# Kernel tuning notes

Measured on AMD Instinct MI355X. Metric: run time of the kernel, lower is better.

## Reference

```python
import jax, jax.numpy as jnp
import numpy as np

HIDDEN = 1024
MOE_FF = 512
SHARED_FF = 2816
NUM_EXPERTS = 16
TOP_K = 2
NORM_TOPK = True


def setup_inputs() -> dict:
    key = jax.random.key(0)
    ks = jax.random.split(key, 8)
    s = 0.02
    return {
        "layer_input": jax.random.normal(ks[0], (1, 2048, HIDDEN), dtype=jnp.float32),
        "gate_w": jax.random.normal(ks[1], (NUM_EXPERTS, HIDDEN), dtype=jnp.float32) * s,
        # fused gate_up weight per expert, laid out for x @ W: [E, hidden, 2*moe_ff]
        "w_gate_up": jax.random.normal(ks[2], (NUM_EXPERTS, HIDDEN, 2 * MOE_FF), dtype=jnp.float32) * s,
        # down weight per expert, laid out for h @ W: [E, moe_ff, hidden]
        "w_down": jax.random.normal(ks[3], (NUM_EXPERTS, MOE_FF, HIDDEN), dtype=jnp.float32) * s,
        # shared expert (Qwen2MoeMLP): Linear weights stored torch-style [out, in]
        "shared_w_gate": jax.random.normal(ks[4], (SHARED_FF, HIDDEN), dtype=jnp.float32) * s,
        "shared_w_up": jax.random.normal(ks[5], (SHARED_FF, HIDDEN), dtype=jnp.float32) * s,
        "shared_w_down": jax.random.normal(ks[6], (HIDDEN, SHARED_FF), dtype=jnp.float32) * s,
        "shared_gate_w": jax.random.normal(ks[7], (1, HIDDEN), dtype=jnp.float32) * s,
    }


def reference(layer_input, gate_w, w_gate_up, w_down,
              shared_w_gate, shared_w_up, shared_w_down, shared_gate_w):
    B, S, D = layer_input.shape
    x = layer_input.reshape(-1, D)  # [N, D]
    N = x.shape[0]

    # shared expert: silu-gated MLP, scaled by per-token sigmoid gate
    shared = (jax.nn.silu(x @ shared_w_gate.T) * (x @ shared_w_up.T)) @ shared_w_down.T
    shared = shared * jax.nn.sigmoid(x @ shared_gate_w.T)  # [N, D]

    # router: softmax in float32, top-k, optional renorm
    logits = x @ gate_w.T  # [N, E]
    probs = jax.nn.softmax(logits.astype(jnp.float32), axis=-1)
    rw, sel = jax.lax.top_k(probs, TOP_K)  # [N, K]
    if NORM_TOPK:
        rw = rw / rw.sum(axis=-1, keepdims=True)
    rw = rw.astype(x.dtype)

    # dense combine weights: zero for unselected experts (equivalent to
    # the sort/dispatch + grouped-GEMM + weighted scatter-combine)
    combine = jnp.zeros((N, NUM_EXPERTS), x.dtype).at[jnp.arange(N)[:, None], sel].set(rw)

    # expert gate_up projection, SwiGLU, down projection, weighted combine
    gu = jnp.einsum('nd,edf->nef', x, w_gate_up)  # [N, E, 2*moe_ff]
    g, h = jnp.split(gu, 2, axis=-1)
    h = jax.nn.silu(g) * h  # [N, E, moe_ff]
    expert_out = jnp.einsum('nef,efd,ne->nd', h, w_down, combine)  # [N, D]

    out = expert_out + shared
    return out.reshape(B, S, D)
```

## Files before the change

kernel.cpp:

```cpp
#include <hip/hip_runtime.h>
#include <hip/hip_bf16.h>

typedef unsigned short ushort_t;
typedef __bf16 bf16x8 __attribute__((ext_vector_type(8)));
typedef float f32x4 __attribute__((ext_vector_type(4)));

#define N_TOK 2048
#define DH    1024
#define FF    512
#define SFF   2816
#define NE    16

#define BM 128
#define BN 64
#define BK 64
#define LDK 72

__device__ __forceinline__ ushort_t f2bf(float f) {
  unsigned int x = __float_as_uint(f);
  unsigned int lsb = (x >> 16) & 1u;
  x += 0x7fffu + lsb;
  return (ushort_t)(x >> 16);
}
__device__ __forceinline__ float bf2f(ushort_t u) {
  union { unsigned int i; float f; } v; v.i = ((unsigned int)u) << 16; return v.f;
}
__device__ __forceinline__ uint4 cvt8v(const float4 a, const float4 b) {
  union { ushort_t u[8]; uint4 v; } r;
  r.u[0] = f2bf(a.x); r.u[1] = f2bf(a.y); r.u[2] = f2bf(a.z); r.u[3] = f2bf(a.w);
  r.u[4] = f2bf(b.x); r.u[5] = f2bf(b.y); r.u[6] = f2bf(b.z); r.u[7] = f2bf(b.w);
  return r.v;
}
__device__ __forceinline__ uint4 ld_cvt8(const float* __restrict__ p) {
  float4 a = *(const float4*)p;
  float4 b = *(const float4*)(p + 4);
  return cvt8v(a, b);
}

__global__ void transpose_kernel(const float* __restrict__ WGU, const float* __restrict__ WDN,
                                 ushort_t* __restrict__ WGUB, ushort_t* __restrict__ WDNB) {
  __shared__ ushort_t tl[64][72];
  int bid = blockIdx.x;
  const float* src; ushort_t* dst; int K, N, kt, nt;
  if (bid < 4096) {
    int e = bid >> 8, rem = bid & 255; kt = rem >> 4; nt = rem & 15;
    src = WGU + (size_t)e * DH * (2 * FF); dst = WGUB + (size_t)e * (2 * FF) * DH;
    K = DH; N = 2 * FF;
  } else {
    int b2 = bid - 4096;
    int e = b2 >> 7, rem = b2 & 127; kt = rem >> 4; nt = rem & 15;
    src = WDN + (size_t)e * FF * DH; dst = WDNB + (size_t)e * DH * FF;
    K = FF; N = DH;
  }
  int t = threadIdx.x;
  int k0 = kt * 64, n0 = nt * 64;
  int r = t >> 2, c0 = (t & 3) * 16;
  const float* sp = src + (size_t)(k0 + r) * N + n0 + c0;
  #pragma unroll
  for (int q = 0; q < 4; ++q) {
    float4 v = *(const float4*)(sp + q * 4);
    tl[c0 + q * 4 + 0][r] = f2bf(v.x);
    tl[c0 + q * 4 + 1][r] = f2bf(v.y);
    tl[c0 + q * 4 + 2][r] = f2bf(v.z);
    tl[c0 + q * 4 + 3][r] = f2bf(v.w);
  }
  __syncthreads();
  ushort_t* dp = dst + (size_t)(n0 + r) * K + k0 + c0;
  *(uint4*)(dp)     = *(uint4*)&tl[r][c0];
  *(uint4*)(dp + 8) = *(uint4*)&tl[r][c0 + 8];
}

__global__ void router_kernel(const float* __restrict__ X, const float* __restrict__ GW,
                              const float* __restrict__ SGW,
                              int* __restrict__ sel, float* __restrict__ wtk,
                              float* __restrict__ sgate) {
  int wave = threadIdx.x >> 6, lane = threadIdx.x & 63;
  int n = blockIdx.x * 4 + wave;
  const float* x = X + (size_t)n * DH;
  int e = lane & 15, s = lane >> 4;
  const float* gw = GW + (size_t)e * DH;
  float lg = 0.f;
  for (int i = 0; i < 256; ++i) {
    int d = s * 256 + i;
    lg += x[d] * gw[d];
  }
  lg += __shfl_down(lg, 32);
  lg += __shfl_down(lg, 16);

  float gd = 0.f;
  #pragma unroll
  for (int i = 0; i < 16; ++i) {
    int d = lane * 16 + i;
    gd += x[d] * SGW[d];
  }
  #pragma unroll
  for (int off = 32; off >= 1; off >>= 1) gd += __shfl_down(gd, off);

  float l[16];
  #pragma unroll
  for (int i = 0; i < 16; ++i) l[i] = __shfl(lg, i);

  if (lane == 0) {
    int i1 = 0; float v1 = l[0];
    #pragma unroll
    for (int i = 1; i < 16; ++i) if (l[i] > v1) { v1 = l[i]; i1 = i; }
    int i2 = -1; float v2 = -1e30f;
    #pragma unroll
    for (int i = 0; i < 16; ++i) { if (i == i1) continue; if (l[i] > v2) { v2 = l[i]; i2 = i; } }
    float p2 = __expf(v2 - v1);
    float inv = 1.f / (1.f + p2);
    sel[n * 2 + 0] = i1; sel[n * 2 + 1] = i2;
    wtk[n * 2 + 0] = inv; wtk[n * 2 + 1] = p2 * inv;
    sgate[n] = 1.f / (1.f + __expf(-gd));
  }
}

__global__ void scatter_kernel(const int* __restrict__ sel,
                               int* __restrict__ toks, int* __restrict__ slot_of,
                               int* __restrict__ offs) {
  __shared__ int cnt[NE], bas[NE];
  int t = threadIdx.x;
  if (t < NE) cnt[t] = 0;
  __syncthreads();
  for (int i = t; i < N_TOK * 2; i += 256) atomicAdd(&cnt[sel[i]], 1);
  __syncthreads();
  if (t == 0) {
    int s = 0;
    for (int e = 0; e < NE; ++e) { bas[e] = s; offs[e] = s; s += cnt[e]; }
    offs[NE] = s;
  }
  __syncthreads();
  if (t < NE) cnt[t] = 0;
  __syncthreads();
  for (int i = t; i < N_TOK * 2; i += 256) {
    int e = sel[i];
    int p = atomicAdd(&cnt[e], 1);
    int slot = bas[e] + p;
    toks[slot] = i >> 1;
    slot_of[i] = slot;
  }
}

__global__ __launch_bounds__(256, 3) void gateup_kernel(
    const float* __restrict__ X, const ushort_t* __restrict__ WGUB,
    const float* __restrict__ SWG, const float* __restrict__ SWU,
    ushort_t* __restrict__ HX, ushort_t* __restrict__ HS,
    const int* __restrict__ toks, const int* __restrict__ offs) {
  __shared__ __align__(16) ushort_t As[BM][LDK];
  __shared__ __align__(16) ushort_t Bgs[BN][LDK];
  __shared__ __align__(16) ushort_t Bus[BN][LDK];
  const int K = DH, NT = K / BK;

  int bid = blockIdx.x;
  int t = threadIdx.x;
  int wave = t >> 6, lane = t & 63;
  int wm = wave & 1, wn = wave >> 1;
  int qd = lane >> 4, l16 = lane & 15;
  int sr = t >> 3, sc = (t & 7) * 8;

  f32x4 accg[4][2], accu[4][2];
  #pragma unroll
  for (int i = 0; i < 4; ++i)
    #pragma unroll
    for (int j = 0; j < 2; ++j) {
      accg[i][j] = (f32x4){0.f, 0.f, 0.f, 0.f};
      accu[i][j] = (f32x4){0.f, 0.f, 0.f, 0.f};
    }

  int m0, n0, M, base, is_exp;

  if (bid < 704) {
    is_exp = 0; base = 0; M = N_TOK;
    n0 = (bid % 44) * BN; m0 = (bid / 44) * BM;
    const float* arow[4];
    const float *bgrow[2], *burow[2];
    #pragma unroll
    for (int p = 0; p < 4; ++p)
      arow[p] = X + (size_t)(m0 + sr + 32 * p) * K + sc;
    #pragma unroll
    for (int p = 0; p < 2; ++p) {
      bgrow[p] = SWG + (size_t)(n0 + sr + 32 * p) * K + sc;
      burow[p] = SWU + (size_t)(n0 + sr + 32 * p) * K + sc;
    }
    uint4 ar[4], bgr[2], bur[2];
    #pragma unroll
    for (int p = 0; p < 4; ++p) ar[p] = ld_cvt8(arow[p]);
    #pragma unroll
    for (int p = 0; p < 2; ++p) { bgr[p] = ld_cvt8(bgrow[p]); bur[p] = ld_cvt8(burow[p]); }

    for (int kt = 0; kt < NT; ++kt) {
      #pragma unroll
      for (int p = 0; p < 4; ++p)
        *(uint4*)&As[sr + 32 * p][sc] = ar[p];
      #pragma unroll
      for (int p = 0; p < 2; ++p) {
        *(uint4*)&Bgs[sr + 32 * p][sc] = bgr[p];
        *(uint4*)&Bus[sr + 32 * p][sc] = bur[p];
      }
      __syncthreads();
      if (kt + 1 < NT) {
        int ko = (kt + 1) * BK;
        #pragma unroll
        for (int p = 0; p < 4; ++p) ar[p] = ld_cvt8(arow[p] + ko);
        #pragma unroll
        for (int p = 0; p < 2; ++p) { bgr[p] = ld_cvt8(bgrow[p] + ko); bur[p] = ld_cvt8(burow[p] + ko); }
      }
      #pragma unroll
      for (int ks = 0; ks < 2; ++ks) {
        int kk = ks * 32 + qd * 8;
        bf16x8 af[4], bgf[2], buf[2];
        #pragma unroll
        for (int i = 0; i < 4; ++i)
          af[i] = *(const bf16x8*)&As[wm * 64 + i * 16 + l16][kk];
        #pragma unroll
        for (int j = 0; j < 2; ++j) {
          bgf[j] = *(const bf16x8*)&Bgs[wn * 32 + j * 16 + l16][kk];
          buf[j] = *(const bf16x8*)&Bus[wn * 32 + j * 16 + l16][kk];
        }
        #pragma unroll
        for (int i = 0; i < 4; ++i)
          #pragma unroll
          for (int j = 0; j < 2; ++j) {
            accg[i][j] = __builtin_amdgcn_mfma_f32_16x16x32_bf16(af[i], bgf[j], accg[i][j], 0, 0, 0);
            accu[i][j] = __builtin_amdgcn_mfma_f32_16x16x32_bf16(af[i], buf[j], accu[i][j], 0, 0, 0);
          }
      }
      __syncthreads();
    }
  } else {
    is_exp = 1;
    int b2 = bid - 704;
    int e = b2 >> 7, rem = b2 & 127;
    n0 = (rem & 7) * BN; m0 = (rem >> 3) * BM;
    base = offs[e]; M = offs[e + 1] - base;
    if (m0 >= M) return;
    const ushort_t* Wt = WGUB + (size_t)e * (2 * FF) * DH;

    const float* arow[4];
    #pragma unroll
    for (int p = 0; p < 4; ++p) {
      int m = m0 + sr + 32 * p;
      int mm = m < M ? m : (M - 1);
      arow[p] = X + (size_t)toks[base + mm] * K + sc;
    }
    const ushort_t *bgrow[2], *burow[2];
    #pragma unroll
    for (int p = 0; p < 2; ++p) {
      bgrow[p] = Wt + (size_t)(n0 + sr + 32 * p) * DH + sc;
      burow[p] = Wt + (size_t)(FF + n0 + sr + 32 * p) * DH + sc;
    }

    uint4 ar[4], bgr[2], bur[2];
    #pragma unroll
    for (int p = 0; p < 4; ++p) ar[p] = ld_cvt8(arow[p]);
    #pragma unroll
    for (int p = 0; p < 2; ++p) { bgr[p] = *(const uint4*)bgrow[p]; bur[p] = *(const uint4*)burow[p]; }

    for (int kt = 0; kt < NT; ++kt) {
      #pragma unroll
      for (int p = 0; p < 4; ++p)
        *(uint4*)&As[sr + 32 * p][sc] = ar[p];
      #pragma unroll
      for (int p = 0; p < 2; ++p) {
        *(uint4*)&Bgs[sr + 32 * p][sc] = bgr[p];
        *(uint4*)&Bus[sr + 32 * p][sc] = bur[p];
      }
      __syncthreads();
      if (kt + 1 < NT) {
        int ko = (kt + 1) * BK;
        #pragma unroll
        for (int p = 0; p < 4; ++p) ar[p] = ld_cvt8(arow[p] + ko);
        #pragma unroll
        for (int p = 0; p < 2; ++p) { bgr[p] = *(const uint4*)(bgrow[p] + ko); bur[p] = *(const uint4*)(burow[p] + ko); }
      }
      #pragma unroll
      for (int ks = 0; ks < 2; ++ks) {
        int kk = ks * 32 + qd * 8;
        bf16x8 af[4], bgf[2], buf[2];
        #pragma unroll
        for (int i = 0; i < 4; ++i)
          af[i] = *(const bf16x8*)&As[wm * 64 + i * 16 + l16][kk];
        #pragma unroll
        for (int j = 0; j < 2; ++j) {
          bgf[j] = *(const bf16x8*)&Bgs[wn * 32 + j * 16 + l16][kk];
          buf[j] = *(const bf16x8*)&Bus[wn * 32 + j * 16 + l16][kk];
        }
        #pragma unroll
        for (int i = 0; i < 4; ++i)
          #pragma unroll
          for (int j = 0; j < 2; ++j) {
            accg[i][j] = __builtin_amdgcn_mfma_f32_16x16x32_bf16(af[i], bgf[j], accg[i][j], 0, 0, 0);
            accu[i][j] = __builtin_amdgcn_mfma_f32_16x16x32_bf16(af[i], buf[j], accu[i][j], 0, 0, 0);
          }
      }
      __syncthreads();
    }
  }

  #pragma unroll
  for (int i = 0; i < 4; ++i)
    #pragma unroll
    for (int r = 0; r < 4; ++r) {
      int row = wm * 64 + i * 16 + qd * 4 + r;
      #pragma unroll
      for (int j = 0; j < 2; ++j) {
        float g = accg[i][j][r], u = accu[i][j][r];
        float h = g / (1.f + __expf(-g)) * u;
        As[row][wn * 32 + j * 16 + l16] = f2bf(h);
      }
    }
  __syncthreads();
  if (is_exp) {
    #pragma unroll
    for (int p = 0; p < 4; ++p) {
      int m = m0 + sr + 32 * p;
      if (m < M)
        *(uint4*)(HX + (size_t)(base + m) * FF + n0 + sc) = *(uint4*)&As[sr + 32 * p][sc];
    }
  } else {
    #pragma unroll
    for (int p = 0; p < 4; ++p) {
      int m = m0 + sr + 32 * p;
      *(uint4*)(HS + (size_t)m * SFF + n0 + sc) = *(uint4*)&As[sr + 32 * p][sc];
    }
  }
}

__global__ __launch_bounds__(256, 4) void down_kernel(
    const ushort_t* __restrict__ HX, const ushort_t* __restrict__ HS,
    const ushort_t* __restrict__ WDNB, const float* __restrict__ SWD,
    ushort_t* __restrict__ SD0, ushort_t* __restrict__ SD1,
    ushort_t* __restrict__ EXPO, const int* __restrict__ offs) {
  __shared__ __align__(16) ushort_t As[BM][LDK];
  __shared__ __align__(16) ushort_t Bs[BN][LDK];

  int bid = blockIdx.x;
  int t = threadIdx.x;
  int wave = t >> 6, lane = t & 63;
  int wm = wave & 1, wn = wave >> 1;
  int qd = lane >> 4, l16 = lane & 15;
  int sr = t >> 3, sc = (t & 7) * 8;

  f32x4 c[4][2];
  #pragma unroll
  for (int i = 0; i < 4; ++i)
    #pragma unroll
    for (int j = 0; j < 2; ++j) c[i][j] = (f32x4){0.f, 0.f, 0.f, 0.f};

  int m0, n0, M, base_row;
  ushort_t* outp;

  if (bid < 512) {
    int kz = bid >> 8, rem = bid & 255;
    m0 = (rem >> 4) * BM; n0 = (rem & 15) * BN;
    M = N_TOK; base_row = 0;
    const int KC = SFF / 2, NT = KC / BK;
    int kb = kz * KC;
    outp = kz ? SD1 : SD0;

    const ushort_t* arow[4];
    const float* brow[2];
    #pragma unroll
    for (int p = 0; p < 4; ++p)
      arow[p] = HS + (size_t)(m0 + sr + 32 * p) * SFF + kb + sc;
    #pragma unroll
    for (int p = 0; p < 2; ++p)
      brow[p] = SWD + (size_t)(n0 + sr + 32 * p) * SFF + kb + sc;

    uint4 ar[4], br[2];
    #pragma unroll
    for (int p = 0; p < 4; ++p) ar[p] = *(const uint4*)(arow[p]);
    #pragma unroll
    for (int p = 0; p < 2; ++p) br[p] = ld_cvt8(brow[p]);

    for (int kt = 0; kt < NT; ++kt) {
      #pragma unroll
      for (int p = 0; p < 4; ++p)
        *(uint4*)&As[sr + 32 * p][sc] = ar[p];
      #pragma unroll
      for (int p = 0; p < 2; ++p)
        *(uint4*)&Bs[sr + 32 * p][sc] = br[p];
      __syncthreads();
      if (kt + 1 < NT) {
        int ko = (kt + 1) * BK;
        #pragma unroll
        for (int p = 0; p < 4; ++p) ar[p] = *(const uint4*)(arow[p] + ko);
        #pragma unroll
        for (int p = 0; p < 2; ++p) br[p] = ld_cvt8(brow[p] + ko);
      }
      #pragma unroll
      for (int ks = 0; ks < 2; ++ks) {
        int kk = ks * 32 + qd * 8;
        bf16x8 af[4], bf[2];
        #pragma unroll
        for (int i = 0; i < 4; ++i)
          af[i] = *(const bf16x8*)&As[wm * 64 + i * 16 + l16][kk];
        #pragma unroll
        for (int j = 0; j < 2; ++j)
          bf[j] = *(const bf16x8*)&Bs[wn * 32 + j * 16 + l16][kk];
        #pragma unroll
        for (int i = 0; i < 4; ++i)
          #pragma unroll
          for (int j = 0; j < 2; ++j)
            c[i][j] = __builtin_amdgcn_mfma_f32_16x16x32_bf16(af[i], bf[j], c[i][j], 0, 0, 0);
      }
      __syncthreads();
    }
  } else {
    int b2 = bid - 512;
    int e = b2 >> 8, rem = b2 & 255;
    n0 = (rem & 15) * BN; m0 = (rem >> 4) * BM;
    int base = offs[e];
    M = offs[e + 1] - base;
    if (m0 >= M) return;
    base_row = base;
    const int NT = FF / BK;
    const ushort_t* Wd = WDNB + (size_t)e * DH * FF;
    const ushort_t* A = HX + (size_t)base * FF;
    outp = EXPO;

    const ushort_t* arow[4];
    #pragma unroll
    for (int p = 0; p < 4; ++p) {
      int m = m0 + sr + 32 * p;
      int mm = m < M ? m : (M - 1);
      arow[p] = A + (size_t)mm * FF + sc;
    }
    const ushort_t* brow[2];
    #pragma unroll
    for (int p = 0; p < 2; ++p)
      brow[p] = Wd + (size_t)(n0 + sr + 32 * p) * FF + sc;

    uint4 ar[4], br[2];
    #pragma unroll
    for (int p = 0; p < 4; ++p) ar[p] = *(const uint4*)(arow[p]);
    #pragma unroll
    for (int p = 0; p < 2; ++p) br[p] = *(const uint4*)(brow[p]);

    for (int kt = 0; kt < NT; ++kt) {
      #pragma unroll
      for (int p = 0; p < 4; ++p)
        *(uint4*)&As[sr + 32 * p][sc] = ar[p];
      #pragma unroll
      for (int p = 0; p < 2; ++p)
        *(uint4*)&Bs[sr + 32 * p][sc] = br[p];
      __syncthreads();
      if (kt + 1 < NT) {
        int ko = (kt + 1) * BK;
        #pragma unroll
        for (int p = 0; p < 4; ++p) ar[p] = *(const uint4*)(arow[p] + ko);
        #pragma unroll
        for (int p = 0; p < 2; ++p) br[p] = *(const uint4*)(brow[p] + ko);
      }
      #pragma unroll
      for (int ks = 0; ks < 2; ++ks) {
        int kk = ks * 32 + qd * 8;
        bf16x8 af[4], bf[2];
        #pragma unroll
        for (int i = 0; i < 4; ++i)
          af[i] = *(const bf16x8*)&As[wm * 64 + i * 16 + l16][kk];
        #pragma unroll
        for (int j = 0; j < 2; ++j)
          bf[j] = *(const bf16x8*)&Bs[wn * 32 + j * 16 + l16][kk];
        #pragma unroll
        for (int i = 0; i < 4; ++i)
          #pragma unroll
          for (int j = 0; j < 2; ++j)
            c[i][j] = __builtin_amdgcn_mfma_f32_16x16x32_bf16(af[i], bf[j], c[i][j], 0, 0, 0);
      }
      __syncthreads();
    }
  }

  #pragma unroll
  for (int i = 0; i < 4; ++i)
    #pragma unroll
    for (int r = 0; r < 4; ++r) {
      int row = wm * 64 + i * 16 + qd * 4 + r;
      #pragma unroll
      for (int j = 0; j < 2; ++j)
        As[row][wn * 32 + j * 16 + l16] = f2bf(c[i][j][r]);
    }
  __syncthreads();
  #pragma unroll
  for (int p = 0; p < 4; ++p) {
    int m = m0 + sr + 32 * p;
    if (m < M)
      *(uint4*)(outp + (size_t)(base_row + m) * DH + n0 + sc) = *(uint4*)&As[sr + 32 * p][sc];
  }
}

__global__ void combine_kernel(const ushort_t* __restrict__ SD0, const ushort_t* __restrict__ SD1,
                               const ushort_t* __restrict__ EXPO,
                               const float* __restrict__ sgate, const float* __restrict__ wtk,
                               const int* __restrict__ slot_of, float* __restrict__ out) {
  int n = blockIdx.x, t = threadIdx.x;
  float sg = sgate[n];
  float w0 = wtk[n * 2 + 0], w1 = wtk[n * 2 + 1];
  int s0 = slot_of[n * 2 + 0], s1 = slot_of[n * 2 + 1];
  int col = t * 4;
  ushort4 d0 = *(const ushort4*)(SD0 + (size_t)n * DH + col);
  ushort4 d1 = *(const ushort4*)(SD1 + (size_t)n * DH + col);
  ushort4 a  = *(const ushort4*)(EXPO + (size_t)s0 * DH + col);
  ushort4 b  = *(const ushort4*)(EXPO + (size_t)s1 * DH + col);
  float4 o;
  o.x = sg * (bf2f(d0.x) + bf2f(d1.x)) + w0 * bf2f(a.x) + w1 * bf2f(b.x);
  o.y = sg * (bf2f(d0.y) + bf2f(d1.y)) + w0 * bf2f(a.y) + w1 * bf2f(b.y);
  o.z = sg * (bf2f(d0.z) + bf2f(d1.z)) + w0 * bf2f(a.z) + w1 * bf2f(b.z);
  o.w = sg * (bf2f(d0.w) + bf2f(d1.w)) + w0 * bf2f(a.w) + w1 * bf2f(b.w);
  *(float4*)(out + (size_t)n * DH + col) = o;
}

extern "C" void kernel_launch(void* const* d_in, const int* in_sizes, int n_in,
                              void* d_out, int out_size, void* d_ws, size_t ws_size,
                              hipStream_t stream) {
  const float* x    = (const float*)d_in[0];
  const float* gw   = (const float*)d_in[1];
  const float* wgu  = (const float*)d_in[2];
  const float* wdn  = (const float*)d_in[3];
  const float* swg  = (const float*)d_in[4];
  const float* swu  = (const float*)d_in[5];
  const float* swd  = (const float*)d_in[6];
  const float* sgw  = (const float*)d_in[7];
  float* out = (float*)d_out;

  char* ws = (char*)d_ws;
  constexpr size_t OFF_HS   = 0;
  constexpr size_t OFF_HX   = OFF_HS   + (size_t)N_TOK * SFF * 2;
  constexpr size_t OFF_SD0  = OFF_HX   + (size_t)4096 * FF * 2;
  constexpr size_t OFF_SD1  = OFF_SD0  + (size_t)N_TOK * DH * 2;
  constexpr size_t OFF_EXPO = OFF_SD1  + (size_t)N_TOK * DH * 2;
  constexpr size_t OFF_WGUB = OFF_EXPO + (size_t)4096 * DH * 2;
  constexpr size_t OFF_WDNB = OFF_WGUB + (size_t)NE * (2 * FF) * DH * 2;
  constexpr size_t OFF_TOK  = OFF_WDNB + (size_t)NE * DH * FF * 2;
  constexpr size_t OFF_OFFS = OFF_TOK  + 4096 * 4;
  constexpr size_t OFF_SEL  = OFF_OFFS + 32 * 4;
  constexpr size_t OFF_WTK  = OFF_SEL  + 4096 * 4;
  constexpr size_t OFF_SG   = OFF_WTK  + 4096 * 4;
  constexpr size_t OFF_SLOT = OFF_SG   + 2048 * 4;

  ushort_t* hs    = (ushort_t*)(ws + OFF_HS);
  ushort_t* hx    = (ushort_t*)(ws + OFF_HX);
  ushort_t* sd0   = (ushort_t*)(ws + OFF_SD0);
  ushort_t* sd1   = (ushort_t*)(ws + OFF_SD1);
  ushort_t* expo  = (ushort_t*)(ws + OFF_EXPO);
  ushort_t* wgub  = (ushort_t*)(ws + OFF_WGUB);
  ushort_t* wdnb  = (ushort_t*)(ws + OFF_WDNB);
  int*      toks  = (int*)(ws + OFF_TOK);
  int*      offs  = (int*)(ws + OFF_OFFS);
  int*      sel   = (int*)(ws + OFF_SEL);
  float*    wtk   = (float*)(ws + OFF_WTK);
  float*    sgate = (float*)(ws + OFF_SG);
  int*      slot_of = (int*)(ws + OFF_SLOT);

  transpose_kernel<<<4096 + 2048, 256, 0, stream>>>(wgu, wdn, wgub, wdnb);
  router_kernel<<<N_TOK / 4, 256, 0, stream>>>(x, gw, sgw, sel, wtk, sgate);
  scatter_kernel<<<1, 256, 0, stream>>>(sel, toks, slot_of, offs);
  gateup_kernel<<<704 + 2048, 256, 0, stream>>>(x, wgub, swg, swu, hx, hs, toks, offs);
  down_kernel<<<512 + 4096, 256, 0, stream>>>(hx, hs, wdnb, swd, sd0, sd1, expo, offs);
  combine_kernel<<<N_TOK, 256, 0, stream>>>(sd0, sd1, expo, sgate, wtk, slot_of, out);
}
```

Baseline: 460.1 us.

## Pre-convert activations and shared weights to bf16; use nontemporal stores

Adds a convert kernel that casts X and the three shared-expert weight matrices to bf16 once, so the GEMM kernels load bf16 directly instead of reading fp32 and converting in every tile. The old code re-read fp32 X and the shared weights many times across tiles. The gateup kernel's two paths are merged into one main loop. Intermediate and output stores become nontemporal. In exchange it adds an extra kernel launch, a full fp32 read plus bf16 write pass, and more workspace.

```diff
diff --git a/kernel.cpp b/kernel.cpp
--- a/kernel.cpp
+++ b/kernel.cpp
@@ -4,6 +4,7 @@
 typedef unsigned short ushort_t;
 typedef __bf16 bf16x8 __attribute__((ext_vector_type(8)));
 typedef float f32x4 __attribute__((ext_vector_type(4)));
+typedef unsigned int u32x4 __attribute__((ext_vector_type(4)));
 
 #define N_TOK 2048
 #define DH    1024
@@ -35,6 +36,25 @@
   float4 a = *(const float4*)p;
   float4 b = *(const float4*)(p + 4);
   return cvt8v(a, b);
+}
+__device__ __forceinline__ void nt_store(ushort_t* p, uint4 v) {
+  union { uint4 h; u32x4 n; } u; u.h = v;
+  __builtin_nontemporal_store(u.n, (u32x4*)p);
+}
+
+__global__ void convert_kernel(const float* __restrict__ X, const float* __restrict__ SWG,
+                               const float* __restrict__ SWU, const float* __restrict__ SWD,
+                               ushort_t* __restrict__ XB, ushort_t* __restrict__ SWGB,
+                               ushort_t* __restrict__ SWUB, ushort_t* __restrict__ SWDB) {
+  const int NX = N_TOK * DH / 8;
+  const int NS = SFF * DH / 8;
+  int i = blockIdx.x * 256 + threadIdx.x;
+  const float* s; ushort_t* d; int off;
+  if (i < NX)               { s = X;   d = XB;   off = i; }
+  else if (i < NX + NS)     { s = SWG; d = SWGB; off = i - NX; }
+  else if (i < NX + 2 * NS) { s = SWU; d = SWUB; off = i - NX - NS; }
+  else                      { s = SWD; d = SWDB; off = i - NX - 2 * NS; }
+  nt_store(d + (size_t)off * 8, ld_cvt8(s + (size_t)off * 8));
 }
 
 __global__ void transpose_kernel(const float* __restrict__ WGU, const float* __restrict__ WDN,
@@ -66,8 +86,8 @@
   }
   __syncthreads();
   ushort_t* dp = dst + (size_t)(n0 + r) * K + k0 + c0;
-  *(uint4*)(dp)     = *(uint4*)&tl[r][c0];
-  *(uint4*)(dp + 8) = *(uint4*)&tl[r][c0 + 8];
+  nt_store(dp,     *(uint4*)&tl[r][c0]);
+  nt_store(dp + 8, *(uint4*)&tl[r][c0 + 8]);
 }
 
 __global__ void router_kernel(const float* __restrict__ X, const float* __restrict__ GW,
@@ -142,8 +162,8 @@
 }
 
 __global__ __launch_bounds__(256, 3) void gateup_kernel(
-    const float* __restrict__ X, const ushort_t* __restrict__ WGUB,
-    const float* __restrict__ SWG, const float* __restrict__ SWU,
+    const ushort_t* __restrict__ XB, const ushort_t* __restrict__ WGUB,
+    const ushort_t* __restrict__ SWGB, const ushort_t* __restrict__ SWUB,
     ushort_t* __restrict__ HX, ushort_t* __restrict__ HS,
     const int* __restrict__ toks, const int* __restrict__ offs) {
   __shared__ __align__(16) ushort_t As[BM][LDK];
@@ -168,64 +188,19 @@
     }
 
   int m0, n0, M, base, is_exp;
+  const ushort_t* arow[4];
+  const ushort_t *bgrow[2], *burow[2];
 
   if (bid < 704) {
     is_exp = 0; base = 0; M = N_TOK;
     n0 = (bid % 44) * BN; m0 = (bid / 44) * BM;
-    const float* arow[4];
-    const float *bgrow[2], *burow[2];
     #pragma unroll
     for (int p = 0; p < 4; ++p)
-      arow[p] = X + (size_t)(m0 + sr + 32 * p) * K + sc;
+      arow[p] = XB + (size_t)(m0 + sr + 32 * p) * K + sc;
     #pragma unroll
     for (int p = 0; p < 2; ++p) {
-      bgrow[p] = SWG + (size_t)(n0 + sr + 32 * p) * K + sc;
-      burow[p] = SWU + (size_t)(n0 + sr + 32 * p) * K + sc;
-    }
-    uint4 ar[4], bgr[2], bur[2];
-    #pragma unroll
-    for (int p = 0; p < 4; ++p) ar[p] = ld_cvt8(arow[p]);
-    #pragma unroll
-    for (int p = 0; p < 2; ++p) { bgr[p] = ld_cvt8(bgrow[p]); bur[p] = ld_cvt8(burow[p]); }
-
-    for (int kt = 0; kt < NT; ++kt) {
-      #pragma unroll
-      for (int p = 0; p < 4; ++p)
-        *(uint4*)&As[sr + 32 * p][sc] = ar[p];
-      #pragma unroll
-      for (int p = 0; p < 2; ++p) {
-        *(uint4*)&Bgs[sr + 32 * p][sc] = bgr[p];
-        *(uint4*)&Bus[sr + 32 * p][sc] = bur[p];
-      }
-      __syncthreads();
-      if (kt + 1 < NT) {
-        int ko = (kt + 1) * BK;
-        #pragma unroll
-        for (int p = 0; p < 4; ++p) ar[p] = ld_cvt8(arow[p] + ko);
-        #pragma unroll
-        for (int p = 0; p < 2; ++p) { bgr[p] = ld_cvt8(bgrow[p] + ko); bur[p] = ld_cvt8(burow[p] + ko); }
-      }
-      #pragma unroll
-      for (int ks = 0; ks < 2; ++ks) {
-        int kk = ks * 32 + qd * 8;
-        bf16x8 af[4], bgf[2], buf[2];
-        #pragma unroll
-        for (int i = 0; i < 4; ++i)
-          af[i] = *(const bf16x8*)&As[wm * 64 + i * 16 + l16][kk];
-        #pragma unroll
-        for (int j = 0; j < 2; ++j) {
-          bgf[j] = *(const bf16x8*)&Bgs[wn * 32 + j * 16 + l16][kk];
-          buf[j] = *(const bf16x8*)&Bus[wn * 32 + j * 16 + l16][kk];
-        }
-        #pragma unroll
-        for (int i = 0; i < 4; ++i)
-          #pragma unroll
-          for (int j = 0; j < 2; ++j) {
-            accg[i][j] = __builtin_amdgcn_mfma_f32_16x16x32_bf16(af[i], bgf[j], accg[i][j], 0, 0, 0);
-            accu[i][j] = __builtin_amdgcn_mfma_f32_16x16x32_bf16(af[i], buf[j], accu[i][j], 0, 0, 0);
-          }
-      }
-      __syncthreads();
+      bgrow[p] = SWGB + (size_t)(n0 + sr + 32 * p) * K + sc;
+      burow[p] = SWUB + (size_t)(n0 + sr + 32 * p) * K + sc;
     }
   } else {
     is_exp = 1;
@@ -235,66 +210,63 @@
     base = offs[e]; M = offs[e + 1] - base;
     if (m0 >= M) return;
     const ushort_t* Wt = WGUB + (size_t)e * (2 * FF) * DH;
-
-    const float* arow[4];
     #pragma unroll
     for (int p = 0; p < 4; ++p) {
       int m = m0 + sr + 32 * p;
       int mm = m < M ? m : (M - 1);
-      arow[p] = X + (size_t)toks[base + mm] * K + sc;
-    }
-    const ushort_t *bgrow[2], *burow[2];
+      arow[p] = XB + (size_t)toks[base + mm] * K + sc;
+    }
     #pragma unroll
     for (int p = 0; p < 2; ++p) {
       bgrow[p] = Wt + (size_t)(n0 + sr + 32 * p) * DH + sc;
       burow[p] = Wt + (size_t)(FF + n0 + sr + 32 * p) * DH + sc;
     }
-
-    uint4 ar[4], bgr[2], bur[2];
-    #pragma unroll
-    for (int p = 0; p < 4; ++p) ar[p] = ld_cvt8(arow[p]);
-    #pragma unroll
-    for (int p = 0; p < 2; ++p) { bgr[p] = *(const uint4*)bgrow[p]; bur[p] = *(const uint4*)burow[p]; }
-
-    for (int kt = 0; kt < NT; ++kt) {
-      #pragma unroll
-      for (int p = 0; p < 4; ++p)
-        *(uint4*)&As[sr + 32 * p][sc] = ar[p];
-      #pragma unroll
-      for (int p = 0; p < 2; ++p) {
-        *(uint4*)&Bgs[sr + 32 * p][sc] = bgr[p];
-        *(uint4*)&Bus[sr + 32 * p][sc] = bur[p];
+  }
+
+  uint4 ar[4], bgr[2], bur[2];
+  #pragma unroll
+  for (int p = 0; p < 4; ++p) ar[p] = *(const uint4*)arow[p];
+  #pragma unroll
+  for (int p = 0; p < 2; ++p) { bgr[p] = *(const uint4*)bgrow[p]; bur[p] = *(const uint4*)burow[p]; }
+
+  for (int kt = 0; kt < NT; ++kt) {
+    #pragma unroll
+    for (int p = 0; p < 4; ++p)
+      *(uint4*)&As[sr + 32 * p][sc] = ar[p];
+    #pragma unroll
+    for (int p = 0; p < 2; ++p) {
+      *(uint4*)&Bgs[sr + 32 * p][sc] = bgr[p];
+      *(uint4*)&Bus[sr + 32 * p][sc] = bur[p];
+    }
+    __syncthreads();
+    if (kt + 1 < NT) {
+      int ko = (kt + 1) * BK;
+      #pragma unroll
+      for (int p = 0; p < 4; ++p) ar[p] = *(const uint4*)(arow[p] + ko);
+      #pragma unroll
+      for (int p = 0; p < 2; ++p) { bgr[p] = *(const uint4*)(bgrow[p] + ko); bur[p] = *(const uint4*)(burow[p] + ko); }
+    }
+    #pragma unroll
+    for (int ks = 0; ks < 2; ++ks) {
+      int kk = ks * 32 + qd * 8;
+      bf16x8 af[4], bgf[2], buf[2];
+      #pragma unroll
+      for (int i = 0; i < 4; ++i)
+        af[i] = *(const bf16x8*)&As[wm * 64 + i * 16 + l16][kk];
+      #pragma unroll
+      for (int j = 0; j < 2; ++j) {
+        bgf[j] = *(const bf16x8*)&Bgs[wn * 32 + j * 16 + l16][kk];
+        buf[j] = *(const bf16x8*)&Bus[wn * 32 + j * 16 + l16][kk];
       }
-      __syncthreads();
-      if (kt + 1 < NT) {
-        int ko = (kt + 1) * BK;
-        #pragma unroll
-        for (int p = 0; p < 4; ++p) ar[p] = ld_cvt8(arow[p] + ko);
-        #pragma unroll
-        for (int p = 0; p < 2; ++p) { bgr[p] = *(const uint4*)(bgrow[p] + ko); bur[p] = *(const uint4*)(burow[p] + ko); }
-      }
-      #pragma unroll
-      for (int ks = 0; ks < 2; ++ks) {
-        int kk = ks * 32 + qd * 8;
-        bf16x8 af[4], bgf[2], buf[2];
-        #pragma unroll
-        for (int i = 0; i < 4; ++i)
-          af[i] = *(const bf16x8*)&As[wm * 64 + i * 16 + l16][kk];
+      #pragma unroll
+      for (int i = 0; i < 4; ++i)
         #pragma unroll
         for (int j = 0; j < 2; ++j) {
-          bgf[j] = *(const bf16x8*)&Bgs[wn * 32 + j * 16 + l16][kk];
-          buf[j] = *(const bf16x8*)&Bus[wn * 32 + j * 16 + l16][kk];
+          accg[i][j] = __builtin_amdgcn_mfma_f32_16x16x32_bf16(af[i], bgf[j], accg[i][j], 0, 0, 0);
+          accu[i][j] = __builtin_amdgcn_mfma_f32_16x16x32_bf16(af[i], buf[j], accu[i][j], 0, 0, 0);
         }
-        #pragma unroll
-        for (int i = 0; i < 4; ++i)
-          #pragma unroll
-          for (int j = 0; j < 2; ++j) {
-            accg[i][j] = __builtin_amdgcn_mfma_f32_16x16x32_bf16(af[i], bgf[j], accg[i][j], 0, 0, 0);
-            accu[i][j] = __builtin_amdgcn_mfma_f32_16x16x32_bf16(af[i], buf[j], accu[i][j], 0, 0, 0);
-          }
-      }
-      __syncthreads();
-    }
+    }
+    __syncthreads();
   }
 
   #pragma unroll
@@ -315,20 +287,20 @@
     for (int p = 0; p < 4; ++p) {
       int m = m0 + sr + 32 * p;
       if (m < M)
-        *(uint4*)(HX + (size_t)(base + m) * FF + n0 + sc) = *(uint4*)&As[sr + 32 * p][sc];
+        nt_store(HX + (size_t)(base + m) * FF + n0 + sc, *(uint4*)&As[sr + 32 * p][sc]);
     }
   } else {
     #pragma unroll
     for (int p = 0; p < 4; ++p) {
       int m = m0 + sr + 32 * p;
-      *(uint4*)(HS + (size_t)m * SFF + n0 + sc) = *(uint4*)&As[sr + 32 * p][sc];
+      nt_store(HS + (size_t)m * SFF + n0 + sc, *(uint4*)&As[sr + 32 * p][sc]);
     }
   }
 }
 
 __global__ __launch_bounds__(256, 4) void down_kernel(
     const ushort_t* __restrict__ HX, const ushort_t* __restrict__ HS,
-    const ushort_t* __restrict__ WDNB, const float* __restrict__ SWD,
+    const ushort_t* __restrict__ WDNB, const ushort_t* __restrict__ SWDB,
     ushort_t* __restrict__ SD0, ushort_t* __restrict__ SD1,
     ushort_t* __restrict__ EXPO, const int* __restrict__ offs) {
   __shared__ __align__(16) ushort_t As[BM][LDK];
@@ -359,19 +331,19 @@
     outp = kz ? SD1 : SD0;
 
     const ushort_t* arow[4];
-    const float* brow[2];
+    const ushort_t* brow[2];
     #pragma unroll
     for (int p = 0; p < 4; ++p)
       arow[p] = HS + (size_t)(m0 + sr + 32 * p) * SFF + kb + sc;
     #pragma unroll
     for (int p = 0; p < 2; ++p)
-      brow[p] = SWD + (size_t)(n0 + sr + 32 * p) * SFF + kb + sc;
+      brow[p] = SWDB + (size_t)(n0 + sr + 32 * p) * SFF + kb + sc;
 
     uint4 ar[4], br[2];
     #pragma unroll
     for (int p = 0; p < 4; ++p) ar[p] = *(const uint4*)(arow[p]);
     #pragma unroll
-    for (int p = 0; p < 2; ++p) br[p] = ld_cvt8(brow[p]);
+    for (int p = 0; p < 2; ++p) br[p] = *(const uint4*)(brow[p]);
 
     for (int kt = 0; kt < NT; ++kt) {
       #pragma unroll
@@ -386,7 +358,7 @@
         #pragma unroll
         for (int p = 0; p < 4; ++p) ar[p] = *(const uint4*)(arow[p] + ko);
         #pragma unroll
-        for (int p = 0; p < 2; ++p) br[p] = ld_cvt8(brow[p] + ko);
+        for (int p = 0; p < 2; ++p) br[p] = *(const uint4*)(brow[p] + ko);
       }
       #pragma unroll
       for (int ks = 0; ks < 2; ++ks) {
@@ -486,7 +458,7 @@
   for (int p = 0; p < 4; ++p) {
     int m = m0 + sr + 32 * p;
     if (m < M)
-      *(uint4*)(outp + (size_t)(base_row + m) * DH + n0 + sc) = *(uint4*)&As[sr + 32 * p][sc];
+      nt_store(outp + (size_t)(base_row + m) * DH + n0 + sc, *(uint4*)&As[sr + 32 * p][sc]);
   }
 }
 
@@ -532,7 +504,11 @@
   constexpr size_t OFF_EXPO = OFF_SD1  + (size_t)N_TOK * DH * 2;
   constexpr size_t OFF_WGUB = OFF_EXPO + (size_t)4096 * DH * 2;
   constexpr size_t OFF_WDNB = OFF_WGUB + (size_t)NE * (2 * FF) * DH * 2;
-  constexpr size_t OFF_TOK  = OFF_WDNB + (size_t)NE * DH * FF * 2;
+  constexpr size_t OFF_XB   = OFF_WDNB + (size_t)NE * DH * FF * 2;
+  constexpr size_t OFF_SWGB = OFF_XB   + (size_t)N_TOK * DH * 2;
+  constexpr size_t OFF_SWUB = OFF_SWGB + (size_t)SFF * DH * 2;
+  constexpr size_t OFF_SWDB = OFF_SWUB + (size_t)SFF * DH * 2;
+  constexpr size_t OFF_TOK  = OFF_SWDB + (size_t)SFF * DH * 2;
   constexpr size_t OFF_OFFS = OFF_TOK  + 4096 * 4;
   constexpr size_t OFF_SEL  = OFF_OFFS + 32 * 4;
   constexpr size_t OFF_WTK  = OFF_SEL  + 4096 * 4;
@@ -546,6 +522,10 @@
   ushort_t* expo  = (ushort_t*)(ws + OFF_EXPO);
   ushort_t* wgub  = (ushort_t*)(ws + OFF_WGUB);
   ushort_t* wdnb  = (ushort_t*)(ws + OFF_WDNB);
+  ushort_t* xb    = (ushort_t*)(ws + OFF_XB);
+  ushort_t* swgb  = (ushort_t*)(ws + OFF_SWGB);
+  ushort_t* swub  = (ushort_t*)(ws + OFF_SWUB);
+  ushort_t* swdb  = (ushort_t*)(ws + OFF_SWDB);
   int*      toks  = (int*)(ws + OFF_TOK);
   int*      offs  = (int*)(ws + OFF_OFFS);
   int*      sel   = (int*)(ws + OFF_SEL);
@@ -553,10 +533,11 @@
   float*    sgate = (float*)(ws + OFF_SG);
   int*      slot_of = (int*)(ws + OFF_SLOT);
 
+  convert_kernel<<<5248, 256, 0, stream>>>(x, swg, swu, swd, xb, swgb, swub, swdb);
   transpose_kernel<<<4096 + 2048, 256, 0, stream>>>(wgu, wdn, wgub, wdnb);
   router_kernel<<<N_TOK / 4, 256, 0, stream>>>(x, gw, sgw, sel, wtk, sgate);
   scatter_kernel<<<1, 256, 0, stream>>>(sel, toks, slot_of, offs);
-  gateup_kernel<<<704 + 2048, 256, 0, stream>>>(x, wgub, swg, swu, hx, hs, toks, offs);
-  down_kernel<<<512 + 4096, 256, 0, stream>>>(hx, hs, wdnb, swd, sd0, sd1, expo, offs);
+  gateup_kernel<<<704 + 2048, 256, 0, stream>>>(xb, wgub, swgb, swub, hx, hs, toks, offs);
+  down_kernel<<<512 + 4096, 256, 0, stream>>>(hx, hs, wdnb, swdb, sd0, sd1, expo, offs);
   combine_kernel<<<N_TOK, 256, 0, stream>>>(sd0, sd1, expo, sgate, wtk, slot_of, out);
 }
```

Result: slower. 591.8 us (+28.6%).
